# Optimization experiments

Hardware: AMD Instinct MI355X
Metric: run time of the kernel (lower is better)

The kernel has to match this reference:

```python
import jax, jax.numpy as jnp
import numpy as np

B, T, D = 2, 2048, 2048
NH, NKV = 16, 4
HD = D // NH  # 128
BASE, TSL = 10000.0, 1024


def rotary_tables(T, hd, base=BASE, tsl=TSL):
    # Matches Rotary.forward with rd == hd (rd=0 in __init__ -> full head dim).
    ar = jnp.arange(0, hd, 2, dtype=jnp.float32) / hd
    if T <= tsl:
        inv = 1.0 / (base ** ar)
    else:
        # NTK-style rescale; note right-assoc exponent in original torch code:
        # 1/(base * (T/tsl) ** ((rd/(rd-2)) ** ar))
        inv = 1.0 / (base * jnp.power(T / tsl, jnp.power(hd / (hd - 2.0), ar)))
    f = jnp.outer(jnp.arange(T, dtype=jnp.float32), inv)  # [T, hd//2]
    cos = jnp.cos(f)[None, :, None, :]  # [1,T,1,hd//2]
    sin = jnp.sin(f)[None, :, None, :]
    return cos, sin


def apply_rope(x, cos, sin):
    # full-dim rope: split halves, rotate
    h = x.shape[-1] // 2
    x1, x2 = x[..., :h], x[..., h:]
    return jnp.concatenate((x1 * cos + x2 * sin, -x1 * sin + x2 * cos), axis=-1)


def rms_norm(x):
    eps = jnp.finfo(x.dtype).eps
    return x * jax.lax.rsqrt(jnp.mean(x * x, axis=-1, keepdims=True) + eps)


def setup_inputs() -> dict:
    key = jax.random.key(0)
    k0, k1, k2, k3, k4 = jax.random.split(key, 5)
    s = 0.02
    return {
        "x": jax.random.normal(k0, (B, T, D), jnp.float32),
        "qw": jax.random.normal(k1, (NH * HD, D), jnp.float32) * s,
        "kw": jax.random.normal(k2, (NKV * HD, D), jnp.float32) * s,
        "vw": jax.random.normal(k3, (NKV * HD, D), jnp.float32) * s,
        "ow": jax.random.normal(k4, (D, D), jnp.float32) * s,
        "qg": jnp.ones((NH,), jnp.float32),
    }


def reference(x, qw, kw, vw, ow, qg):
    Bx, Tx, Dx = x.shape
    q = (x @ qw.T).reshape(Bx, Tx, NH, HD)
    k = (x @ kw.T).reshape(Bx, Tx, NKV, HD)
    v = (x @ vw.T).reshape(Bx, Tx, NKV, HD)
    q = rms_norm(q)
    k = rms_norm(k)
    cos, sin = rotary_tables(Tx, HD)
    q = apply_rope(q, cos, sin) * qg[None, None, :, None]
    k = apply_rope(k, cos, sin)
    # GQA: repeat kv heads
    r = NH // NKV
    k = jnp.repeat(k, r, axis=2)  # [B,T,NH,HD]
    v = jnp.repeat(v, r, axis=2)
    scale = 1.0 / jnp.sqrt(jnp.asarray(HD, q.dtype))
    scores = jnp.einsum("bqhd,bkhd->bhqk", q, k) * scale  # [B,NH,T,T]
    causal = jnp.tril(jnp.ones((Tx, Tx), dtype=bool))
    scores = jnp.where(causal[None, None, :, :], scores, jnp.asarray(-jnp.inf, scores.dtype))
    attn = jax.nn.softmax(scores, axis=-1)
    y = jnp.einsum("bhqk,bkhd->bqhd", attn, v)  # [B,T,NH,HD]
    return y.reshape(Bx, Tx, Dx) @ ow.T
```

## Files before the change

kernel.cpp:

```cpp
#include <hip/hip_runtime.h>
#include <hip/hip_bf16.h>
#include <stdint.h>


typedef __attribute__((ext_vector_type(8))) short short8;
typedef __attribute__((ext_vector_type(4))) float f32x4;

#define GLOAD16(gp, lp) \
  __builtin_amdgcn_global_load_lds((const __attribute__((address_space(1))) void*)(gp), \
                                   (__attribute__((address_space(3))) void*)(lp), 16, 0, 0)

__device__ __forceinline__ float bf2f(unsigned short u) {
  union { unsigned int i; float f; } v; v.i = ((unsigned int)u) << 16; return v.f;
}
__device__ __forceinline__ unsigned short f2bf(float f) {
  union { float fl; unsigned int i; } v; v.fl = f;
  unsigned int r = v.i + 0x7fffu + ((v.i >> 16) & 1u);
  return (unsigned short)(r >> 16);
}

__global__ __launch_bounds__(256) void prep_kernel(
    const float* __restrict__ x, const float* __restrict__ qw,
    const float* __restrict__ kw, const float* __restrict__ vw,
    const float* __restrict__ ow,
    unsigned short* __restrict__ xb, unsigned short* __restrict__ wqkv,
    unsigned short* __restrict__ owb, float* __restrict__ cost, float* __restrict__ sint) {
  const int NX = 2097152;
  const int NW = 1572864;
  const int NO = 1048576;
  const int NT = 131072;
  int tid = blockIdx.x * 256 + threadIdx.x;
  if (tid < NX) {
    float4 v = ((const float4*)x)[tid];
    uint2 o; o.x = (unsigned)f2bf(v.x) | ((unsigned)f2bf(v.y) << 16);
    o.y = (unsigned)f2bf(v.z) | ((unsigned)f2bf(v.w) << 16);
    ((uint2*)xb)[tid] = o;
  } else if (tid < NX + NW) {
    int i = tid - NX; int e = i * 4;
    const float* src = (e < 4194304) ? (qw + e)
                     : (e < 5242880) ? (kw + (e - 4194304))
                                     : (vw + (e - 5242880));
    float4 v = *(const float4*)src;
    uint2 o; o.x = (unsigned)f2bf(v.x) | ((unsigned)f2bf(v.y) << 16);
    o.y = (unsigned)f2bf(v.z) | ((unsigned)f2bf(v.w) << 16);
    ((uint2*)wqkv)[i] = o;
  } else if (tid < NX + NW + NO) {
    int i = tid - NX - NW;
    float4 v = ((const float4*)ow)[i];
    uint2 o; o.x = (unsigned)f2bf(v.x) | ((unsigned)f2bf(v.y) << 16);
    o.y = (unsigned)f2bf(v.z) | ((unsigned)f2bf(v.w) << 16);
    ((uint2*)owb)[i] = o;
  } else if (tid < NX + NW + NO + NT) {
    int i = tid - NX - NW - NO;
    int t = i >> 6, j = i & 63;
    float e = exp2f(0.02272008f * (float)j * (1.0f / 64.0f));
    float inv = 1.0f / (10000.0f * exp2f(e));
    float f = (float)t * inv;
    cost[i] = cosf(f);
    sint[i] = sinf(f);
  }
}

template <int OUTF>
__global__ __launch_bounds__(512) void gemm_bt2(const unsigned short* __restrict__ A,
                                                const unsigned short* __restrict__ Bw,
                                                void* __restrict__ Cp,
                                                int MT, int NT, int N, int K) {
  extern __shared__ char smc[];
  const int tid = threadIdx.x;
  const int l = tid & 63, w = tid >> 6;
  const int lane_r = l & 15, lane_g = l >> 4;
  const int wr = w >> 1, wc = w & 1;

  int nwg = MT * NT, qch = nwg >> 3;
  int orig = blockIdx.x;
  int wgid = (orig & 7) * qch + (orig >> 3);
  int by = wgid % MT;
  int bx = wgid / MT;
  const int m0 = by * 256, n0 = bx * 128;

  f32x4 acc[4][4];
#pragma unroll
  for (int i = 0; i < 4; ++i)
#pragma unroll
    for (int j = 0; j < 4; ++j) acc[i][j] = {0.f, 0.f, 0.f, 0.f};

  const unsigned short* gA[4]; int lA[4];
#pragma unroll
  for (int t = 0; t < 4; ++t) {
    int idx = t * 512 + tid;
    int row = idx >> 3, c = idx & 7, gc = c ^ (row & 7);
    gA[t] = A + (size_t)(m0 + row) * K + gc * 8;
    lA[t] = idx * 16;
  }
  const unsigned short* gB[2]; int lB[2];
#pragma unroll
  for (int t = 0; t < 2; ++t) {
    int idx = t * 512 + tid;
    int row = idx >> 3, c = idx & 7, gc = c ^ (row & 7);
    gB[t] = Bw + (size_t)(n0 + row) * K + gc * 8;
    lB[t] = idx * 16;
  }
  int oA[4][2], oB[4][2];
#pragma unroll
  for (int i = 0; i < 4; ++i)
#pragma unroll
    for (int ks = 0; ks < 2; ++ks) {
      int ra = wr * 64 + i * 16 + lane_r;
      oA[i][ks] = (ra * 128 + ks * 64 + lane_g * 16) ^ ((ra & 7) << 4);
      int rb = wc * 64 + i * 16 + lane_r;
      oB[i][ks] = (rb * 128 + ks * 64 + lane_g * 16) ^ ((rb & 7) << 4);
    }

  auto STAGE = [&](int kt, int bsel) {
    char* kd = smc + bsel * 49152;
    char* bd = kd + 32768;
#pragma unroll
    for (int t = 0; t < 4; ++t) GLOAD16(gA[t] + kt, kd + lA[t]);
#pragma unroll
    for (int t = 0; t < 2; ++t) GLOAD16(gB[t] + kt, bd + lB[t]);
  };

  const int NS = K >> 6;
  STAGE(0, 0);
  STAGE(64, 1);
#pragma unroll 1
  for (int s = 0; s < NS; ++s) {
    if (s + 1 < NS) asm volatile("s_waitcnt vmcnt(6)" ::: "memory");
    else            asm volatile("s_waitcnt vmcnt(0)" ::: "memory");
    __builtin_amdgcn_s_barrier();
    __builtin_amdgcn_sched_barrier(0);
    if (s + 2 < NS) STAGE((s + 2) * 64, (s + 2) % 3);
    const char* ab = smc + (s % 3) * 49152;
    const char* bb = ab + 32768;
    short8 af[4][2], bf[4][2];
#pragma unroll
    for (int i = 0; i < 4; ++i)
#pragma unroll
      for (int ks = 0; ks < 2; ++ks) {
        af[i][ks] = *(const short8*)(ab + oA[i][ks]);
        bf[i][ks] = *(const short8*)(bb + oB[i][ks]);
      }
    __builtin_amdgcn_s_setprio(1);
#pragma unroll
    for (int i = 0; i < 4; ++i)
#pragma unroll
      for (int j = 0; j < 4; ++j)
#pragma unroll
        for (int ks = 0; ks < 2; ++ks)
          acc[i][j] = __builtin_amdgcn_mfma_f32_16x16x32_bf16(af[i][ks], bf[j][ks], acc[i][j], 0, 0, 0);
    __builtin_amdgcn_s_setprio(0);
  }
#pragma unroll
  for (int i = 0; i < 4; ++i) {
    int row = m0 + wr * 64 + i * 16 + lane_g * 4;
#pragma unroll
    for (int j = 0; j < 4; ++j) {
      int col = n0 + wc * 64 + j * 16 + lane_r;
#pragma unroll
      for (int r = 0; r < 4; ++r) {
        float v = acc[i][j][r];
        if (OUTF)
          ((float*)Cp)[(size_t)(row + r) * N + col] = v;
        else
          ((unsigned short*)Cp)[(size_t)(row + r) * N + col] = f2bf(v);
      }
    }
  }
}

__global__ __launch_bounds__(256) void normrope_kernel(unsigned short* __restrict__ qkv,
                                                       const float* __restrict__ cost,
                                                       const float* __restrict__ sint,
                                                       const float* __restrict__ qg) {
  const int tid = threadIdx.x, l = tid & 63, w = tid >> 6;
  int row = blockIdx.x * 4 + w;
  int tok = row / 20, hh = row - tok * 20;
  int t = tok & 2047;
  bool isq = hh < 16;
  int col0 = isq ? hh * 128 : 2048 + (hh - 16) * 128;
  unsigned short* p = qkv + (size_t)tok * 3072 + col0 + 2 * l;
  unsigned int u = *(const unsigned int*)p;
  float x0 = bf2f((unsigned short)(u & 0xffffu));
  float x1 = bf2f((unsigned short)(u >> 16));
  float ss = x0 * x0 + x1 * x1;
#pragma unroll
  for (int m = 1; m < 64; m <<= 1) ss += __shfl_xor(ss, m);
  float rn = rsqrtf(ss * (1.0f / 128.0f) + 1.1920928955078125e-07f);
  float n0 = x0 * rn, n1 = x1 * rn;
  float p0 = __shfl_xor(n0, 32);
  float p1 = __shfl_xor(n1, 32);
  int jj = (2 * l) & 63;
  float c0 = cost[t * 64 + jj], c1 = cost[t * 64 + jj + 1];
  float s0 = sint[t * 64 + jj], s1 = sint[t * 64 + jj + 1];
  float o0, o1;
  if (l < 32) { o0 = n0 * c0 + p0 * s0; o1 = n1 * c1 + p1 * s1; }
  else        { o0 = -p0 * s0 + n0 * c0; o1 = -p1 * s1 + n1 * c1; }
  if (isq) { float g = qg[hh] * 0.08838834764831845f; o0 *= g; o1 *= g; }
  *(unsigned int*)p = (unsigned)f2bf(o0) | ((unsigned)f2bf(o1) << 16);
}

__global__ __launch_bounds__(256) void vtrans_kernel(const unsigned short* __restrict__ qkv,
                                                     unsigned short* __restrict__ vtg) {
  __shared__ unsigned short tile[64][132];
  int bid = blockIdx.x;
  int pan = bid & 7, tt = bid >> 3;
  int b = pan >> 2, kvh = pan & 3;
  int t0 = tt * 64;
  const unsigned short* src = qkv + ((size_t)(b * 2048 + t0)) * 3072 + 2560 + kvh * 128;
#pragma unroll
  for (int i = 0; i < 8; ++i) {
    int idx = i * 256 + threadIdx.x;
    int row = idx >> 5, c4 = idx & 31;
    uint2 v = *(const uint2*)(src + (size_t)row * 3072 + c4 * 4);
    *(uint2*)&tile[row][c4 * 4] = v;
  }
  __syncthreads();
  unsigned short* dst = vtg + (size_t)pan * 262144 + t0;
#pragma unroll
  for (int i = 0; i < 8; ++i) {
    int idx = i * 256 + threadIdx.x;
    int d = idx >> 4, tc = idx & 15;
    unsigned short a0 = tile[tc * 4 + 0][d], a1 = tile[tc * 4 + 1][d];
    unsigned short a2 = tile[tc * 4 + 2][d], a3 = tile[tc * 4 + 3][d];
    uint2 o; o.x = (unsigned)a0 | ((unsigned)a1 << 16);
    o.y = (unsigned)a2 | ((unsigned)a3 << 16);
    *(uint2*)(dst + (size_t)d * 2048 + tc * 4) = o;
  }
}

__global__ __launch_bounds__(512) void attn_fa4(const unsigned short* __restrict__ qkv,
                                                const unsigned short* __restrict__ vtg,
                                                unsigned short* __restrict__ y) {
  extern __shared__ char smc[];
  const int tid = threadIdx.x;
  const int l = tid & 63, w = tid >> 6;
  const int lane_r = l & 15, lane_g = l >> 4;

  int n = blockIdx.x;
  int pan = n & 7;
  int b = pan >> 2, kvh = pan & 3;
  int idx2 = n >> 3;
  int h = kvh * 4 + (idx2 & 3);
  int pairIdx = idx2 >> 2;
  const size_t rowbase = (size_t)b * 2048;
  const unsigned short* kvK = qkv + rowbase * 3072;
  const unsigned short* vtp = vtg + (size_t)pan * 262144;

  int kg[2], vg[2], sl[2];
#pragma unroll
  for (int t = 0; t < 2; ++t) {
    int idx = t * 512 + tid;
    { int row = idx >> 4, c = idx & 15, gc = c ^ (row & 7);
      kg[t] = row * 3072 + 2048 + kvh * 128 + gc * 8; }
    { int d = idx >> 3, c = idx & 7, gc = c ^ (d & 7);
      vg[t] = d * 2048 + gc * 8; }
    sl[t] = idx * 16;
  }
  const int swz = (lane_r & 7) << 4;
  int oK[4][4];
#pragma unroll
  for (int ct = 0; ct < 4; ++ct)
#pragma unroll
    for (int ks = 0; ks < 4; ++ks)
      oK[ct][ks] = ((ct * 16 + lane_r) * 256 + ks * 64 + lane_g * 16) ^ swz;
  int oV[2][8];
#pragma unroll
  for (int kk = 0; kk < 2; ++kk)
#pragma unroll
    for (int dt = 0; dt < 8; ++dt)
      oV[kk][dt] = ((dt * 16 + lane_r) * 128 + kk * 64 + lane_g * 16) ^ swz;
  const int pbase = 65536 + w * 2048;
  int pw_off[4];
#pragma unroll
  for (int ct = 0; ct < 4; ++ct)
    pw_off[ct] = pbase + lane_r * 128 + ((ct * 32 + lane_g * 8) ^ swz);
  int pr_off[2];
#pragma unroll
  for (int kk = 0; kk < 2; ++kk)
    pr_off[kk] = pbase + lane_r * 128 + ((kk * 64 + lane_g * 16) ^ swz);

  auto STAGE = [&](int tile, int bufsel) {
    const unsigned short* srcK = kvK + (size_t)tile * 64 * 3072;
    const unsigned short* srcV = vtp + tile * 64;
    char* kd = smc + bufsel * 16384;
    char* vd = smc + 32768 + bufsel * 16384;
#pragma unroll
    for (int t = 0; t < 2; ++t) {
      GLOAD16(srcK + kg[t], kd + sl[t]);
      GLOAD16(srcV + vg[t], vd + sl[t]);
    }
  };

#pragma unroll 1
  for (int phase = 0; phase < 2; ++phase) {
    const int qt = phase ? pairIdx : 15 - pairIdx;
    const int q0 = qt * 128;
    const int nkb = 2 * qt + 2;
    const int wrow0 = q0 + w * 16;
    const int qrow = wrow0 + lane_r;

    STAGE(0, 0);
    short8 qf[4];
#pragma unroll
    for (int ks = 0; ks < 4; ++ks)
      qf[ks] = *(const short8*)(qkv + (rowbase + qrow) * 3072 + h * 128 + ks * 32 + lane_g * 8);

    f32x4 acc[8];
#pragma unroll
    for (int dt = 0; dt < 8; ++dt) acc[dt] = {0.f, 0.f, 0.f, 0.f};
    float mrun = -1e30f, lrun = 0.f;

    __syncthreads();

#pragma unroll 1
    for (int kb = 0; kb < nkb; ++kb) {
      const int cur = kb & 1;
      if (kb + 1 < nkb) STAGE(kb + 1, cur ^ 1);
      const int j0 = kb * 64;
      const bool active = (j0 <= wrow0 + 15);
      if (active) {
        const int kbb = cur * 16384;
        f32x4 s[4];
#pragma unroll
        for (int ct = 0; ct < 4; ++ct) s[ct] = {0.f, 0.f, 0.f, 0.f};
        __builtin_amdgcn_s_setprio(1);
#pragma unroll
        for (int ct = 0; ct < 4; ++ct)
#pragma unroll
          for (int ks = 0; ks < 4; ++ks) {
            short8 kf = *(const short8*)(smc + kbb + oK[ct][ks]);
            s[ct] = __builtin_amdgcn_mfma_f32_16x16x32_bf16(kf, qf[ks], s[ct], 0, 0, 0);
          }
        __builtin_amdgcn_s_setprio(0);
        if (j0 + 63 > wrow0) {
#pragma unroll
          for (int ct = 0; ct < 4; ++ct) {
            int kg0 = j0 + ct * 16 + lane_g * 4;
#pragma unroll
            for (int r = 0; r < 4; ++r)
              if (kg0 + r > qrow) s[ct][r] = -1e30f;
          }
        }
        float mx = s[0][0];
#pragma unroll
        for (int ct = 0; ct < 4; ++ct)
#pragma unroll
          for (int r = 0; r < 4; ++r) mx = fmaxf(mx, s[ct][r]);
        mx = fmaxf(mx, __shfl_xor(mx, 16));
        mx = fmaxf(mx, __shfl_xor(mx, 32));
        float mn = fmaxf(mrun, mx);
        float corr = __expf(mrun - mn);
        mrun = mn;
        float rs = 0.f;
#pragma unroll
        for (int ct = 0; ct < 4; ++ct)
#pragma unroll
          for (int r = 0; r < 4; ++r) {
            float e = __expf(s[ct][r] - mn);
            s[ct][r] = e; rs += e;
          }
        rs += __shfl_xor(rs, 16);
        rs += __shfl_xor(rs, 32);
        lrun = lrun * corr + rs;
#pragma unroll
        for (int ct = 0; ct < 4; ++ct) {
          uint2 pv;
          pv.x = (unsigned)f2bf(s[ct][0]) | ((unsigned)f2bf(s[ct][1]) << 16);
          pv.y = (unsigned)f2bf(s[ct][2]) | ((unsigned)f2bf(s[ct][3]) << 16);
          *(uint2*)(smc + pw_off[ct]) = pv;
        }
#pragma unroll
        for (int dt = 0; dt < 8; ++dt)
#pragma unroll
          for (int r = 0; r < 4; ++r) acc[dt][r] *= corr;
        short8 pf[2];
        pf[0] = *(const short8*)(smc + pr_off[0]);
        pf[1] = *(const short8*)(smc + pr_off[1]);
        const int vbase = 32768 + cur * 16384;
        __builtin_amdgcn_s_setprio(1);
#pragma unroll
        for (int kk = 0; kk < 2; ++kk)
#pragma unroll
          for (int dt = 0; dt < 8; ++dt) {
            short8 vf = *(const short8*)(smc + vbase + oV[kk][dt]);
            acc[dt] = __builtin_amdgcn_mfma_f32_16x16x32_bf16(vf, pf[kk], acc[dt], 0, 0, 0);
          }
        __builtin_amdgcn_s_setprio(0);
      }
      __syncthreads();
    }
    float linv = 1.0f / lrun;
    unsigned short* yrow = y + (rowbase + qrow) * 2048 + h * 128;
#pragma unroll
    for (int dt = 0; dt < 8; ++dt) {
      uint2 o;
      o.x = (unsigned)f2bf(acc[dt][0] * linv) | ((unsigned)f2bf(acc[dt][1] * linv) << 16);
      o.y = (unsigned)f2bf(acc[dt][2] * linv) | ((unsigned)f2bf(acc[dt][3] * linv) << 16);
      *(uint2*)(yrow + dt * 16 + lane_g * 4) = o;
    }
  }
}

extern "C" void kernel_launch(void* const* d_in, const int* in_sizes, int n_in,
                              void* d_out, int out_size, void* d_ws, size_t ws_size,
                              hipStream_t stream) {
  (void)in_sizes; (void)n_in; (void)out_size; (void)ws_size;
  const float* x  = (const float*)d_in[0];
  const float* qw = (const float*)d_in[1];
  const float* kw = (const float*)d_in[2];
  const float* vw = (const float*)d_in[3];
  const float* ow = (const float*)d_in[4];
  const float* qg = (const float*)d_in[5];

  char* ws = (char*)d_ws;
  unsigned short* xb   = (unsigned short*)(ws + 0);
  unsigned short* vtg  = (unsigned short*)(ws + 0);
  unsigned short* wqkv = (unsigned short*)(ws + 16777216);
  unsigned short* owb  = (unsigned short*)(ws + 29360128);
  unsigned short* qkvb = (unsigned short*)(ws + 37748736);
  unsigned short* y    = (unsigned short*)(ws + 62914560);
  float* cost          = (float*)(ws + 79691776);
  float* sint          = (float*)(ws + 80216064);

  prep_kernel<<<18944, 256, 0, stream>>>(x, qw, kw, vw, ow, xb, wqkv, owb, cost, sint);
  gemm_bt2<0><<<384, 512, 147456, stream>>>(xb, wqkv, qkvb, 16, 24, 3072, 2048);
  normrope_kernel<<<20480, 256, 0, stream>>>(qkvb, cost, sint, qg);
  vtrans_kernel<<<256, 256, 0, stream>>>(qkvb, vtg);
  attn_fa4<<<256, 512, 81920, stream>>>(qkvb, vtg, y);
  gemm_bt2<1><<<256, 512, 147456, stream>>>(y, owb, d_out, 16, 16, 2048, 2048);
}
```

Measured before the change: 214.4 us.

## Replace GEMM with 256x256 tiles and four-phase quadrant-pipelined loads

Both projection GEMMs now use a new kernel that splits each K-step into four MFMA phases over A/B quadrants. Each phase is separated by a barrier, and the next stage's A and B halves are loaded between phases into a double buffer. The QKV GEMM grows to 256x256 tiles (192 blocks), and the output GEMM uses 128x256 tiles, with a 2x4 warp layout. The goal is to hide global loads behind MFMA work and raise data reuse per tile. The cost is more barriers per step and fewer blocks than the 256 CUs for the QKV GEMM.

After: 200.4 us. 6.5% less time.

```diff
diff --git a/kernel.cpp b/kernel.cpp
--- a/kernel.cpp
+++ b/kernel.cpp
@@ -9,6 +9,8 @@
 #define GLOAD16(gp, lp) \
   __builtin_amdgcn_global_load_lds((const __attribute__((address_space(1))) void*)(gp), \
                                    (__attribute__((address_space(3))) void*)(lp), 16, 0, 0)
+
+#define BAR() do { asm volatile("" ::: "memory"); __builtin_amdgcn_s_barrier(); asm volatile("" ::: "memory"); } while (0)
 
 __device__ __forceinline__ float bf2f(unsigned short u) {
   union { unsigned int i; float f; } v; v.i = ((unsigned int)u) << 16; return v.f;
@@ -61,112 +63,161 @@
   }
 }
 
-template <int OUTF>
-__global__ __launch_bounds__(512) void gemm_bt2(const unsigned short* __restrict__ A,
-                                                const unsigned short* __restrict__ Bw,
-                                                void* __restrict__ Cp,
-                                                int MT, int NT, int N, int K) {
+template <int IM, int OUTF>
+__global__ __launch_bounds__(512) void gemm8ph(const unsigned short* __restrict__ A,
+                                               const unsigned short* __restrict__ Bw,
+                                               void* __restrict__ Cp,
+                                               int MT, int NTn, int N, int K) {
   extern __shared__ char smc[];
+  constexpr int S = IM * 8;
+  constexpr int IQ = IM / 2;
+  constexpr int ASZ = IM * 2048;
+  constexpr int DB = 2 * ASZ + 32768;
+  constexpr int AL = (IM * 128) / 512;
   const int tid = threadIdx.x;
   const int l = tid & 63, w = tid >> 6;
   const int lane_r = l & 15, lane_g = l >> 4;
-  const int wr = w >> 1, wc = w & 1;
-
-  int nwg = MT * NT, qch = nwg >> 3;
+  const int wr = w >> 2, wc = w & 3;
+
+  int qch = (MT * NTn) >> 3;
   int orig = blockIdx.x;
   int wgid = (orig & 7) * qch + (orig >> 3);
-  int by = wgid % MT;
-  int bx = wgid / MT;
-  const int m0 = by * 256, n0 = bx * 128;
-
-  f32x4 acc[4][4];
-#pragma unroll
-  for (int i = 0; i < 4; ++i)
+  int by = wgid / NTn, bx = wgid - by * NTn;
+  const int m0 = by * IM * 32, n0 = bx * 256;
+
+  f32x4 acc[IM][4];
+#pragma unroll
+  for (int i = 0; i < IM; ++i)
 #pragma unroll
     for (int j = 0; j < 4; ++j) acc[i][j] = {0.f, 0.f, 0.f, 0.f};
 
-  const unsigned short* gA[4]; int lA[4];
-#pragma unroll
-  for (int t = 0; t < 4; ++t) {
+  const unsigned short* srcA[AL]; int ldA[AL];
+#pragma unroll
+  for (int t = 0; t < AL; ++t) {
     int idx = t * 512 + tid;
-    int row = idx >> 3, c = idx & 7, gc = c ^ (row & 7);
-    gA[t] = A + (size_t)(m0 + row) * K + gc * 8;
-    lA[t] = idx * 16;
-  }
-  const unsigned short* gB[2]; int lB[2];
+    int rc = idx >> 3, kc = idx & 7;
+    int wrp = rc >= S ? 1 : 0, rr = rc & (S - 1);
+    int row = wrp * 2 * S + rr;
+    srcA[t] = A + (size_t)(m0 + row) * K + (kc ^ (rc & 7)) * 8;
+    ldA[t] = idx * 16;
+  }
+  const unsigned short* srcB[2]; int ldB[2];
 #pragma unroll
   for (int t = 0; t < 2; ++t) {
     int idx = t * 512 + tid;
-    int row = idx >> 3, c = idx & 7, gc = c ^ (row & 7);
-    gB[t] = Bw + (size_t)(n0 + row) * K + gc * 8;
-    lB[t] = idx * 16;
-  }
-  int oA[4][2], oB[4][2];
-#pragma unroll
-  for (int i = 0; i < 4; ++i)
+    int rc = idx >> 3, kc = idx & 7;
+    int nrow = (rc >> 5) * 64 + (rc & 31);
+    srcB[t] = Bw + (size_t)(n0 + nrow) * K + (kc ^ (rc & 7)) * 8;
+    ldB[t] = idx * 16;
+  }
+  const int SK = S * K, JK = 32 * K;
+
+  auto STA = [&](int kt, int ih, int dqb) {
+    char* d = smc + dqb + ih * ASZ;
+#pragma unroll
+    for (int t = 0; t < AL; ++t) GLOAD16(srcA[t] + kt + ih * SK, d + ldA[t]);
+  };
+  auto STB = [&](int kt, int jh, int dqb) {
+    char* d = smc + dqb + 2 * ASZ + jh * 16384;
+#pragma unroll
+    for (int t = 0; t < 2; ++t) GLOAD16(srcB[t] + kt + jh * JK, d + ldB[t]);
+  };
+
+  int oA[IQ][2], oB[2][2];
+#pragma unroll
+  for (int iq = 0; iq < IQ; ++iq)
 #pragma unroll
     for (int ks = 0; ks < 2; ++ks) {
-      int ra = wr * 64 + i * 16 + lane_r;
-      oA[i][ks] = (ra * 128 + ks * 64 + lane_g * 16) ^ ((ra & 7) << 4);
-      int rb = wc * 64 + i * 16 + lane_r;
-      oB[i][ks] = (rb * 128 + ks * 64 + lane_g * 16) ^ ((rb & 7) << 4);
-    }
-
-  auto STAGE = [&](int kt, int bsel) {
-    char* kd = smc + bsel * 49152;
-    char* bd = kd + 32768;
-#pragma unroll
-    for (int t = 0; t < 4; ++t) GLOAD16(gA[t] + kt, kd + lA[t]);
-#pragma unroll
-    for (int t = 0; t < 2; ++t) GLOAD16(gB[t] + kt, bd + lB[t]);
-  };
+      int rc = wr * S + iq * 16 + lane_r;
+      oA[iq][ks] = rc * 128 + ((ks * 64 + lane_g * 16) ^ ((rc & 7) << 4));
+    }
+#pragma unroll
+  for (int jj = 0; jj < 2; ++jj)
+#pragma unroll
+    for (int ks = 0; ks < 2; ++ks) {
+      int rc = wc * 32 + jj * 16 + lane_r;
+      oB[jj][ks] = rc * 128 + ((ks * 64 + lane_g * 16) ^ ((rc & 7) << 4));
+    }
+
+#define VMC() do { if constexpr (IM == 8) asm volatile("s_waitcnt vmcnt(6)" ::: "memory"); \
+                   else                   asm volatile("s_waitcnt vmcnt(5)" ::: "memory"); } while (0)
+#define VM0() asm volatile("s_waitcnt vmcnt(0)" ::: "memory")
+#define MM(IH, JH, BR) do { \
+    __builtin_amdgcn_s_setprio(1); \
+    _Pragma("unroll") \
+    for (int iq = 0; iq < IQ; ++iq) \
+      _Pragma("unroll") \
+      for (int jj = 0; jj < 2; ++jj) \
+        _Pragma("unroll") \
+        for (int ks = 0; ks < 2; ++ks) \
+          acc[(IH) * IQ + iq][(JH) * 2 + jj] = __builtin_amdgcn_mfma_f32_16x16x32_bf16( \
+              af[iq][ks], BR[jj][ks], acc[(IH) * IQ + iq][(JH) * 2 + jj], 0, 0, 0); \
+    __builtin_amdgcn_s_setprio(0); } while (0)
 
   const int NS = K >> 6;
-  STAGE(0, 0);
-  STAGE(64, 1);
+  STA(0, 0, 0); STB(0, 0, 0); STB(0, 1, 0); STA(0, 1, 0);
+  STA(64, 0, DB); STB(64, 0, DB); STB(64, 1, DB);
+  VMC();
+  BAR();
+
 #pragma unroll 1
   for (int s = 0; s < NS; ++s) {
-    if (s + 1 < NS) asm volatile("s_waitcnt vmcnt(6)" ::: "memory");
-    else            asm volatile("s_waitcnt vmcnt(0)" ::: "memory");
-    __builtin_amdgcn_s_barrier();
-    __builtin_amdgcn_sched_barrier(0);
-    if (s + 2 < NS) STAGE((s + 2) * 64, (s + 2) % 3);
-    const char* ab = smc + (s % 3) * 49152;
-    const char* bb = ab + 32768;
-    short8 af[4][2], bf[4][2];
-#pragma unroll
-    for (int i = 0; i < 4; ++i)
-#pragma unroll
-      for (int ks = 0; ks < 2; ++ks) {
-        af[i][ks] = *(const short8*)(ab + oA[i][ks]);
-        bf[i][ks] = *(const short8*)(bb + oB[i][ks]);
+    const int dq = (s & 1) * DB, dn = DB - dq;
+    const char* Ab = smc + dq;
+    const char* Bb = Ab + 2 * ASZ;
+    short8 af[IQ][2], b0[2][2], b1[2][2];
+    if (s + 1 < NS) STA((s + 1) << 6, 1, dn);
+#pragma unroll
+    for (int iq = 0; iq < IQ; ++iq)
+#pragma unroll
+      for (int ks = 0; ks < 2; ++ks) af[iq][ks] = *(const short8*)(Ab + oA[iq][ks]);
+#pragma unroll
+    for (int jj = 0; jj < 2; ++jj)
+#pragma unroll
+      for (int ks = 0; ks < 2; ++ks) b0[jj][ks] = *(const short8*)(Bb + oB[jj][ks]);
+    MM(0, 0, b0);
+    BAR();
+    if (s + 2 < NS) STA((s + 2) << 6, 0, dq);
+#pragma unroll
+    for (int jj = 0; jj < 2; ++jj)
+#pragma unroll
+      for (int ks = 0; ks < 2; ++ks) b1[jj][ks] = *(const short8*)(Bb + 16384 + oB[jj][ks]);
+    MM(0, 1, b1);
+    BAR();
+    if (s + 2 < NS) STB((s + 2) << 6, 0, dq);
+#pragma unroll
+    for (int iq = 0; iq < IQ; ++iq)
+#pragma unroll
+      for (int ks = 0; ks < 2; ++ks) af[iq][ks] = *(const short8*)(Ab + ASZ + oA[iq][ks]);
+    MM(1, 0, b0);
+    BAR();
+    if (s + 2 < NS) STB((s + 2) << 6, 1, dq);
+    MM(1, 1, b1);
+    if (s + 2 < NS) VMC(); else VM0();
+    BAR();
+  }
+#undef VMC
+#undef VM0
+#undef MM
+
+#pragma unroll
+  for (int ih = 0; ih < 2; ++ih)
+#pragma unroll
+    for (int iq = 0; iq < IQ; ++iq) {
+      int row = m0 + wr * 2 * S + ih * S + iq * 16 + lane_g * 4;
+#pragma unroll
+      for (int j = 0; j < 4; ++j) {
+        int col = n0 + wc * 64 + j * 16 + lane_r;
+#pragma unroll
+        for (int r = 0; r < 4; ++r) {
+          float v = acc[ih * IQ + iq][j][r];
+          if (OUTF)
+            ((float*)Cp)[(size_t)(row + r) * N + col] = v;
+          else
+            ((unsigned short*)Cp)[(size_t)(row + r) * N + col] = f2bf(v);
+        }
       }
-    __builtin_amdgcn_s_setprio(1);
-#pragma unroll
-    for (int i = 0; i < 4; ++i)
-#pragma unroll
-      for (int j = 0; j < 4; ++j)
-#pragma unroll
-        for (int ks = 0; ks < 2; ++ks)
-          acc[i][j] = __builtin_amdgcn_mfma_f32_16x16x32_bf16(af[i][ks], bf[j][ks], acc[i][j], 0, 0, 0);
-    __builtin_amdgcn_s_setprio(0);
-  }
-#pragma unroll
-  for (int i = 0; i < 4; ++i) {
-    int row = m0 + wr * 64 + i * 16 + lane_g * 4;
-#pragma unroll
-    for (int j = 0; j < 4; ++j) {
-      int col = n0 + wc * 64 + j * 16 + lane_r;
-#pragma unroll
-      for (int r = 0; r < 4; ++r) {
-        float v = acc[i][j][r];
-        if (OUTF)
-          ((float*)Cp)[(size_t)(row + r) * N + col] = v;
-        else
-          ((unsigned short*)Cp)[(size_t)(row + r) * N + col] = f2bf(v);
-      }
-    }
-  }
+    }
 }
 
 __global__ __launch_bounds__(256) void normrope_kernel(unsigned short* __restrict__ qkv,
@@ -424,9 +475,9 @@
   float* sint          = (float*)(ws + 80216064);
 
   prep_kernel<<<18944, 256, 0, stream>>>(x, qw, kw, vw, ow, xb, wqkv, owb, cost, sint);
-  gemm_bt2<0><<<384, 512, 147456, stream>>>(xb, wqkv, qkvb, 16, 24, 3072, 2048);
+  gemm8ph<8, 0><<<192, 512, 131072, stream>>>(xb, wqkv, qkvb, 16, 12, 3072, 2048);
   normrope_kernel<<<20480, 256, 0, stream>>>(qkvb, cost, sint, qg);
   vtrans_kernel<<<256, 256, 0, stream>>>(qkvb, vtg);
   attn_fa4<<<256, 512, 81920, stream>>>(qkvb, vtg, y);
-  gemm_bt2<1><<<256, 512, 147456, stream>>>(y, owb, d_out, 16, 16, 2048, 2048);
-}
+  gemm8ph<4, 1><<<256, 512, 98304, stream>>>(y, owb, d_out, 32, 8, 2048, 2048);
+}
```
